# Performance work log

Measured on AMD Instinct MI355X. Metric: run time of the kernel, lower is better.

## Reference

```python
import jax, jax.numpy as jnp
import numpy as np

N = 25600          # total nodes
B = 64             # graphs in batch
NPG = N // B       # nodes per graph (400)
K = 16             # in-degree (regular graph)
E = N * K          # edges
D = 128            # hidden dim = out dim
L = 4              # DGN layers
NUM_ATOM = 128


def _linear_init(key, out_s, in_s):
    lim = 1.0 / np.sqrt(in_s)
    return jax.random.uniform(key, (out_s, in_s), jnp.float32, -lim, lim)


def setup_inputs() -> dict:
    key = jax.random.key(0)
    ks = jax.random.split(key, 16)
    node_feat = jax.random.randint(ks[0], (N,), 0, NUM_ATOM)
    # K-regular in-degree graph, edges intra-graph; dst sorted
    dst = jnp.repeat(jnp.arange(N), K)                       # [E]
    src_local = jax.random.randint(ks[1], (E,), 0, NPG)
    src = (dst // NPG) * NPG + src_local                     # same graph as dst
    eig = jax.random.normal(ks[2], (E, 2), jnp.float32)
    snorm_n = jnp.full((N, 1), 1.0 / np.sqrt(NPG), jnp.float32)
    graph_ids = jnp.arange(N) // NPG
    emb = jax.random.normal(ks[3], (NUM_ATOM, D), jnp.float32) * 0.02
    pre_W = jnp.stack([_linear_init(jax.random.fold_in(ks[4], i), D, 2 * D) for i in range(L)])
    pre_b = jnp.zeros((L, D), jnp.float32)
    post_W = jnp.stack([_linear_init(jax.random.fold_in(ks[5], i), D, 5 * D) for i in range(L)])
    post_b = jnp.zeros((L, D), jnp.float32)
    r_W0 = _linear_init(ks[6], 64, 128); r_b0 = jnp.zeros((64,), jnp.float32)
    r_W1 = _linear_init(ks[7], 32, 64);  r_b1 = jnp.zeros((32,), jnp.float32)
    r_W2 = _linear_init(ks[8], 128, 32); r_b2 = jnp.zeros((128,), jnp.float32)
    return dict(node_feat=node_feat, src=src, dst=dst, eig=eig, snorm_n=snorm_n,
                graph_ids=graph_ids, emb=emb, pre_W=pre_W, pre_b=pre_b,
                post_W=post_W, post_b=post_b, r_W0=r_W0, r_b0=r_b0,
                r_W1=r_W1, r_b1=r_b1, r_W2=r_W2, r_b2=r_b2)


def _dgn_layer(h, src, dst, eig, snorm_n, Wp, bp, Wq, bq):
    n = h.shape[0]
    # pretrans on edges: Linear(cat(h_src, h_dst))  [E, D]
    z2 = jnp.concatenate([h[src], h[dst]], axis=-1)
    e = jnp.einsum('ei,oi->eo', z2, Wp) + bp
    seg_sum = lambda v: jax.ops.segment_sum(v, dst, num_segments=n, indices_are_sorted=True)
    s = seg_sum(e)
    mean = s / K
    mx = jax.ops.segment_max(e, dst, num_segments=n, indices_are_sorted=True)
    # directional aggregator (eig_idx=1)
    w = eig[:, 1]
    denom = seg_sum(jnp.abs(w)) + 1e-8                       # [n]
    ew = w / denom[dst]                                      # [E]
    dir_agg = jnp.abs(seg_sum(e * ew[:, None]) - seg_sum(ew)[:, None] * h)
    agg = jnp.concatenate([h, mean, s, mx, dir_agg], axis=-1)  # [n, 5D]
    hn = jnp.einsum('ni,oi->no', agg, Wq) + bq
    hn = hn * snorm_n           # graph_norm
    hn = jax.nn.relu(hn)
    return h + hn               # residual (in_dim == out_dim)


def reference(node_feat, src, dst, eig, snorm_n, graph_ids, emb,
              pre_W, pre_b, post_W, post_b,
              r_W0, r_b0, r_W1, r_b1, r_W2, r_b2):
    h = emb[node_feat]                                       # AtomEncoder
    for i in range(L):
        h = _dgn_layer(h, src, dst, eig, snorm_n, pre_W[i], pre_b[i], post_W[i], post_b[i])
    # mean_nodes per graph (equal-sized graphs)
    hg = jax.ops.segment_sum(h, graph_ids, num_segments=B, indices_are_sorted=True) / NPG
    y = jax.nn.relu(hg @ r_W0.T + r_b0)
    y = jax.nn.relu(y @ r_W1.T + r_b1)
    return y @ r_W2.T + r_b2                                 # [B, 128]
```

## Files before the change

### kernel.cpp

```cpp
#include <hip/hip_runtime.h>
#include <cstddef>

#define NN 25600
#define BB 64
#define NPG 400
#define KK 16
#define LL 4

typedef _Float16 half_t;
typedef _Float16 h8 __attribute__((ext_vector_type(8)));
typedef _Float16 h4 __attribute__((ext_vector_type(4)));
typedef _Float16 h2 __attribute__((ext_vector_type(2)));
typedef float f32x4 __attribute__((ext_vector_type(4)));

__global__ __launch_bounds__(256) void prep_k(const float* __restrict__ preW,
                                              const float* __restrict__ preb,
                                              const float* __restrict__ postW,
                                              half_t* __restrict__ WpreH,
                                              half_t* __restrict__ WpreL,
                                              float* __restrict__ bpre,
                                              half_t* __restrict__ WpostH,
                                              half_t* __restrict__ WpostL) {
  int idx = blockIdx.x * 256 + threadIdx.x;
  const int n1 = LL * 256 * 128;
  const int n2 = n1 + LL * 256;
  const int n3 = n2 + LL * 128 * 512;
  if (idx < n1) {
    int l = idx / 32768;
    int q = idx % 32768;
    int j = q & 7, lane = (q >> 3) & 63, kc = (q >> 9) & 3, c16 = q >> 11;
    int col = c16 * 16 + (lane & 15);
    int k = kc * 32 + (lane >> 4) * 8 + j;
    float v = (col < 128) ? preW[(size_t)l * 32768 + (size_t)col * 256 + k]
                          : preW[(size_t)l * 32768 + (size_t)(col - 128) * 256 + 128 + k];
    half_t hi = (half_t)v;
    WpreH[idx] = hi;
    WpreL[idx] = (half_t)(v - (float)hi);
  } else if (idx < n2) {
    int r = idx - n1;
    int l = r / 256, o = r % 256;
    bpre[r] = (o < 128) ? 0.f : preb[l * 128 + (o - 128)];
  } else if (idx < n3) {
    int r = idx - n2;
    int l = r / 65536;
    int q = r % 65536;
    int j = q & 7, lane = (q >> 3) & 63, kc = (q >> 9) & 15, c16 = q >> 13;
    int col = c16 * 16 + (lane & 15);
    int k = kc * 32 + (lane >> 4) * 8 + j;
    int jblk = k >> 7, kk = k & 127;
    const float* base = postW + (size_t)l * 128 * 640 + (size_t)col * 640;
    float v;
    if (jblk == 0)      v = base[kk];
    else if (jblk == 1) v = base[128 + kk] * (1.f / 16.f) + base[256 + kk];
    else if (jblk == 2) v = base[384 + kk];
    else                v = base[512 + kk];
    half_t hi = (half_t)v;
    WpostH[r] = hi;
    WpostL[r] = (half_t)(v - (float)hi);
  }
}

__global__ __launch_bounds__(256) void embed_k(const int* __restrict__ nf,
                                               const float* __restrict__ emb,
                                               float* __restrict__ hf,
                                               half_t* __restrict__ Hh,
                                               half_t* __restrict__ Hl) {
  int idx = blockIdx.x * 256 + threadIdx.x;
  int n = idx >> 5;
  int d4 = idx & 31;
  int a = nf[n];
  float4 v = *(const float4*)(emb + (size_t)a * 128 + d4 * 4);
  *(float4*)(hf + (size_t)n * 128 + d4 * 4) = v;
  h4 hi, lo;
  const float* vp = &v.x;
#pragma unroll
  for (int j = 0; j < 4; ++j) {
    half_t h = (half_t)vp[j];
    hi[j] = h;
    lo[j] = (half_t)(vp[j] - (float)h);
  }
  *(h4*)(Hh + (size_t)n * 128 + d4 * 4) = hi;
  *(h4*)(Hl + (size_t)n * 128 + d4 * 4) = lo;
}

__global__ __launch_bounds__(256) void pre_gemm_k(const half_t* __restrict__ Ah_g,
                                                  const half_t* __restrict__ Al_g,
                                                  const half_t* __restrict__ Wh_g,
                                                  const half_t* __restrict__ Wl_g,
                                                  const float* __restrict__ bias,
                                                  float* __restrict__ outF) {
  __shared__ half_t Ahs[64][132];
  __shared__ half_t Als[64][132];
  const int tid = threadIdx.x;
  const int bid = blockIdx.x;
  const int swz = (bid & 7) * 50 + (bid >> 3);
  const int r0 = swz * 64;
  const int by8 = blockIdx.y * 8;
  const int wid = tid >> 6, lane = tid & 63;
  const int wm = wid >> 1, wn = wid & 1;
  const int lr = lane & 15, lk = (lane >> 4) * 8;
  f32x4 acc[2][4] = {};

  {
    const int row = tid >> 2;
#pragma unroll
    for (int s = 0; s < 4; ++s) {
      const int koff = (tid & 3) * 8 + s * 32;
      const size_t g = (size_t)(r0 + row) * 128 + koff;
      *(h8*)&Ahs[row][koff] = *(const h8*)(Ah_g + g);
      *(h8*)&Als[row][koff] = *(const h8*)(Al_g + g);
    }
  }
  __syncthreads();

#pragma unroll
  for (int kc = 0; kc < 4; ++kc) {
    h8 af[2][2];
#pragma unroll
    for (int mi = 0; mi < 2; ++mi) {
      const int r = wm * 32 + mi * 16 + lr;
      af[mi][0] = *(const h8*)&Ahs[r][kc * 32 + lk];
      af[mi][1] = *(const h8*)&Als[r][kc * 32 + lk];
    }
#pragma unroll
    for (int nj = 0; nj < 4; ++nj) {
      const size_t fi = ((size_t)((by8 + wn * 4 + nj) * 4 + kc) * 64 + lane) * 8;
      const h8 b0v = *(const h8*)(Wh_g + fi);
      const h8 b1v = *(const h8*)(Wl_g + fi);
#pragma unroll
      for (int mi = 0; mi < 2; ++mi) {
        acc[mi][nj] = __builtin_amdgcn_mfma_f32_16x16x32_f16(af[mi][0], b0v, acc[mi][nj], 0, 0, 0);
        acc[mi][nj] = __builtin_amdgcn_mfma_f32_16x16x32_f16(af[mi][0], b1v, acc[mi][nj], 0, 0, 0);
        acc[mi][nj] = __builtin_amdgcn_mfma_f32_16x16x32_f16(af[mi][1], b0v, acc[mi][nj], 0, 0, 0);
      }
    }
  }
#pragma unroll
  for (int mi = 0; mi < 2; ++mi) {
    const int rowb = r0 + wm * 32 + mi * 16 + (lane >> 4) * 4;
#pragma unroll
    for (int nj = 0; nj < 4; ++nj) {
      const int col = by8 * 16 + wn * 64 + nj * 16 + lr;
      const float bv = bias[col];
#pragma unroll
      for (int q = 0; q < 4; ++q) {
        outF[(size_t)(rowb + q) * 256 + col] = acc[mi][nj][q] + bv;
      }
    }
  }
}

__global__ __launch_bounds__(256) void agg_post_k(const float* __restrict__ pre,
                                                  const int* __restrict__ src,
                                                  const float* __restrict__ eig,
                                                  const half_t* __restrict__ Hh,
                                                  const half_t* __restrict__ Hl,
                                                  const half_t* __restrict__ Wh,
                                                  const half_t* __restrict__ Wl,
                                                  const float* __restrict__ bias,
                                                  const float* __restrict__ snorm,
                                                  float* __restrict__ Hf,
                                                  half_t* __restrict__ Oh,
                                                  half_t* __restrict__ Ol) {
  __shared__ half_t Ah[16][392];
  __shared__ half_t Al[16][392];
  const int tid = threadIdx.x;
  const int bid = blockIdx.x;
  const int swz = (bid & 7) * 200 + (bid >> 3);
  const int r0 = swz * 16;
  const int wid = tid >> 6, lane = tid & 63;
  const int wn = wid;
  const int lr = lane & 15, lk = (lane >> 4) * 8;

  for (int i = 0; i < 4; ++i) {
    const int lrow = wid * 4 + i;
    const int n = r0 + lrow;
    int sv[KK];
    float wv[KK];
    {
      const int4* sp4 = (const int4*)(src + (size_t)n * KK);
      const float4* ep4 = (const float4*)(eig + (size_t)n * KK * 2);
#pragma unroll
      for (int t = 0; t < 4; ++t) {
        const int4 s4 = sp4[t];
        sv[4 * t + 0] = s4.x;
        sv[4 * t + 1] = s4.y;
        sv[4 * t + 2] = s4.z;
        sv[4 * t + 3] = s4.w;
      }
#pragma unroll
      for (int t = 0; t < 8; ++t) {
        const float4 e4 = ep4[t];
        wv[2 * t + 0] = e4.y;
        wv[2 * t + 1] = e4.w;
      }
    }
    float denom = 0.f;
#pragma unroll
    for (int e = 0; e < KK; ++e) denom += fabsf(wv[e]);
    denom += 1e-8f;
    const float inv = 1.f / denom;
    float sum_ew = 0.f;
#pragma unroll
    for (int e = 0; e < KK; ++e) {
      wv[e] *= inv;
      sum_ew += wv[e];
    }
    float sA0 = 0.f, sA1 = 0.f, wA0 = 0.f, wA1 = 0.f;
    float mA0 = -3.402823466e+38f, mA1 = -3.402823466e+38f;
#pragma unroll
    for (int e = 0; e < KK; ++e) {
      const float2 a = *(const float2*)(pre + (size_t)sv[e] * 256 + 2 * lane);
      sA0 += a.x;
      sA1 += a.y;
      wA0 = fmaf(wv[e], a.x, wA0);
      wA1 = fmaf(wv[e], a.y, wA1);
      mA0 = fmaxf(mA0, a.x);
      mA1 = fmaxf(mA1, a.y);
    }
    const float2 b = *(const float2*)(pre + (size_t)n * 256 + 128 + 2 * lane);
    const float2 hv = *(const float2*)(Hf + (size_t)n * 128 + 2 * lane);
    const int d0 = 2 * lane;
    auto wr2 = [&](int kcol, float v0, float v1) {
      h2 hi, lo;
      hi[0] = (half_t)v0;
      hi[1] = (half_t)v1;
      lo[0] = (half_t)(v0 - (float)hi[0]);
      lo[1] = (half_t)(v1 - (float)hi[1]);
      *(h2*)&Ah[lrow][kcol] = hi;
      *(h2*)&Al[lrow][kcol] = lo;
    };
    wr2(d0, sA0 + 16.f * b.x, sA1 + 16.f * b.y);
    wr2(128 + d0, mA0 + b.x, mA1 + b.y);
    wr2(256 + d0, fabsf(wA0 + sum_ew * (b.x - hv.x)), fabsf(wA1 + sum_ew * (b.y - hv.y)));
  }

  const int frow = r0 + lr;
  h8 afh[4][2];
#pragma unroll
  for (int hc = 0; hc < 4; ++hc) {
    afh[hc][0] = *(const h8*)(Hh + (size_t)frow * 128 + hc * 32 + lk);
    afh[hc][1] = *(const h8*)(Hl + (size_t)frow * 128 + hc * 32 + lk);
  }

  __syncthreads();

  f32x4 acc[2] = {};
#pragma unroll
  for (int kc = 0; kc < 16; ++kc) {
    h8 a0, a1;
    if (kc < 4) {
      a0 = afh[kc & 3][0];
      a1 = afh[kc & 3][1];
    } else {
      a0 = *(const h8*)&Ah[lr][(kc - 4) * 32 + lk];
      a1 = *(const h8*)&Al[lr][(kc - 4) * 32 + lk];
    }
#pragma unroll
    for (int nj = 0; nj < 2; ++nj) {
      const size_t fi = ((size_t)((wn * 2 + nj) * 16 + kc) * 64 + lane) * 8;
      const h8 b0v = *(const h8*)(Wh + fi);
      const h8 b1v = *(const h8*)(Wl + fi);
      acc[nj] = __builtin_amdgcn_mfma_f32_16x16x32_f16(a0, b0v, acc[nj], 0, 0, 0);
      acc[nj] = __builtin_amdgcn_mfma_f32_16x16x32_f16(a0, b1v, acc[nj], 0, 0, 0);
      acc[nj] = __builtin_amdgcn_mfma_f32_16x16x32_f16(a1, b0v, acc[nj], 0, 0, 0);
    }
  }

  const int rowb = r0 + (lane >> 4) * 4;
#pragma unroll
  for (int nj = 0; nj < 2; ++nj) {
    const int col = wn * 32 + nj * 16 + lr;
    const float bv = bias[col];
#pragma unroll
    for (int q = 0; q < 4; ++q) {
      const int r = rowb + q;
      float a = acc[nj][q] + bv;
      a *= snorm[r];
      a = fmaxf(a, 0.f);
      const float hn = Hf[(size_t)r * 128 + col] + a;
      Hf[(size_t)r * 128 + col] = hn;
      const half_t hi = (half_t)hn;
      Oh[(size_t)r * 128 + col] = hi;
      Ol[(size_t)r * 128 + col] = (half_t)(hn - (float)hi);
    }
  }
}

__global__ __launch_bounds__(256) void reduce_mlp_k(const float* __restrict__ h,
                                                    const float* __restrict__ W0, const float* __restrict__ b0,
                                                    const float* __restrict__ W1, const float* __restrict__ b1,
                                                    const float* __restrict__ W2, const float* __restrict__ b2,
                                                    float* __restrict__ out) {
  __shared__ float hgs[128];
  __shared__ float red[128];
  __shared__ float y0s[64];
  __shared__ float y1s[32];
  __shared__ float wb[64 * 130];
  const int g = blockIdx.x;
  const int t = threadIdx.x;
  {
    const int d = t & 127, hf = t >> 7;
    const float* p = h + ((size_t)g * NPG + (size_t)hf * 200) * 128 + d;
    float acc = 0.f;
    for (int i = 0; i < 200; ++i) acc += p[(size_t)i * 128];
    if (hf) red[d] = acc;
    __syncthreads();
    if (!hf) hgs[d] = (acc + red[d]) * (1.f / (float)NPG);
  }
  __syncthreads();
  for (int idx = t; idx < 64 * 128; idx += 256) {
    wb[(idx >> 7) * 130 + (idx & 127)] = W0[idx];
  }
  __syncthreads();
  if (t < 64) {
    float a = b0[t];
    const float* w = &wb[t * 130];
    for (int k = 0; k < 128; ++k) a = fmaf(hgs[k], w[k], a);
    y0s[t] = fmaxf(a, 0.f);
  }
  __syncthreads();
  for (int idx = t; idx < 32 * 64; idx += 256) {
    wb[(idx >> 6) * 66 + (idx & 63)] = W1[idx];
  }
  __syncthreads();
  if (t < 32) {
    float a = b1[t];
    const float* w = &wb[t * 66];
    for (int k = 0; k < 64; ++k) a = fmaf(y0s[k], w[k], a);
    y1s[t] = fmaxf(a, 0.f);
  }
  __syncthreads();
  for (int idx = t; idx < 128 * 32; idx += 256) {
    wb[(idx >> 5) * 34 + (idx & 31)] = W2[idx];
  }
  __syncthreads();
  if (t < 128) {
    float a = b2[t];
    const float* w = &wb[t * 34];
    for (int k = 0; k < 32; ++k) a = fmaf(y1s[k], w[k], a);
    out[(size_t)g * 128 + t] = a;
  }
}

extern "C" void kernel_launch(void* const* d_in, const int* in_sizes, int n_in,
                              void* d_out, int out_size, void* d_ws, size_t ws_size,
                              hipStream_t stream) {
  const int* node_feat = (const int*)d_in[0];
  const int* src = (const int*)d_in[1];
  const float* eig = (const float*)d_in[3];
  const float* snorm = (const float*)d_in[4];
  const float* emb = (const float*)d_in[6];
  const float* preW = (const float*)d_in[7];
  const float* preb = (const float*)d_in[8];
  const float* postW = (const float*)d_in[9];
  const float* postb = (const float*)d_in[10];
  const float* rW0 = (const float*)d_in[11];
  const float* rb0 = (const float*)d_in[12];
  const float* rW1 = (const float*)d_in[13];
  const float* rb1 = (const float*)d_in[14];
  const float* rW2 = (const float*)d_in[15];
  const float* rb2 = (const float*)d_in[16];
  float* out = (float*)d_out;

  half_t* Hh = (half_t*)d_ws;
  half_t* Hl = Hh + (size_t)NN * 128;
  float* Hf = (float*)(Hl + (size_t)NN * 128);
  float* pre = Hf + (size_t)NN * 128;
  half_t* WpreH = (half_t*)(pre + (size_t)NN * 256);
  half_t* WpreL = WpreH + (size_t)LL * 32768;
  half_t* WpostH = WpreL + (size_t)LL * 32768;
  half_t* WpostL = WpostH + (size_t)LL * 65536;
  float* bpre = (float*)(WpostL + (size_t)LL * 65536);

  prep_k<<<1540, 256, 0, stream>>>(preW, preb, postW, WpreH, WpreL, bpre, WpostH, WpostL);
  embed_k<<<(NN * 32) / 256, 256, 0, stream>>>(node_feat, emb, Hf, Hh, Hl);

  for (int l = 0; l < LL; ++l) {
    pre_gemm_k<<<dim3(NN / 64, 2), 256, 0, stream>>>(
        Hh, Hl, WpreH + (size_t)l * 32768, WpreL + (size_t)l * 32768,
        bpre + (size_t)l * 256, pre);
    agg_post_k<<<NN / 16, 256, 0, stream>>>(
        pre, src, eig, Hh, Hl, WpostH + (size_t)l * 65536, WpostL + (size_t)l * 65536,
        postb + (size_t)l * 128, snorm, Hf, Hh, Hl);
  }

  reduce_mlp_k<<<BB, 256, 0, stream>>>(Hf, rW0, rb0, rW1, rb1, rW2, rb2, out);
}
```

Baseline: 266.0 us.

## Fuse dst-half pretrans GEMM into aggregation and drop fp32 hidden buffer

The pre-GEMM now computes only the source-side 128 columns. Each aggregation block computes the destination-side projection for its own 16 rows with MFMA into shared memory, which halves the size of the intermediate edge-projection buffer in global memory. The fp32 copy of the hidden state is also removed: the residual and the readout reconstruct h from the fp16 hi/lo split, which cuts global reads and writes. The cost is extra MFMA work and shared memory in agg_post_k, plus slightly lower precision for the residual state.

```diff
diff --git a/kernel.cpp b/kernel.cpp
--- a/kernel.cpp
+++ b/kernel.cpp
@@ -62,7 +62,6 @@
 
 __global__ __launch_bounds__(256) void embed_k(const int* __restrict__ nf,
                                                const float* __restrict__ emb,
-                                               float* __restrict__ hf,
                                                half_t* __restrict__ Hh,
                                                half_t* __restrict__ Hl) {
   int idx = blockIdx.x * 256 + threadIdx.x;
@@ -70,7 +69,6 @@
   int d4 = idx & 31;
   int a = nf[n];
   float4 v = *(const float4*)(emb + (size_t)a * 128 + d4 * 4);
-  *(float4*)(hf + (size_t)n * 128 + d4 * 4) = v;
   h4 hi, lo;
   const float* vp = &v.x;
 #pragma unroll
@@ -87,15 +85,13 @@
                                                   const half_t* __restrict__ Al_g,
                                                   const half_t* __restrict__ Wh_g,
                                                   const half_t* __restrict__ Wl_g,
-                                                  const float* __restrict__ bias,
-                                                  float* __restrict__ outF) {
+                                                  float* __restrict__ preA) {
   __shared__ half_t Ahs[64][132];
   __shared__ half_t Als[64][132];
   const int tid = threadIdx.x;
   const int bid = blockIdx.x;
   const int swz = (bid & 7) * 50 + (bid >> 3);
   const int r0 = swz * 64;
-  const int by8 = blockIdx.y * 8;
   const int wid = tid >> 6, lane = tid & 63;
   const int wm = wid >> 1, wn = wid & 1;
   const int lr = lane & 15, lk = (lane >> 4) * 8;
@@ -124,7 +120,7 @@
     }
 #pragma unroll
     for (int nj = 0; nj < 4; ++nj) {
-      const size_t fi = ((size_t)((by8 + wn * 4 + nj) * 4 + kc) * 64 + lane) * 8;
+      const size_t fi = ((size_t)((wn * 4 + nj) * 4 + kc) * 64 + lane) * 8;
       const h8 b0v = *(const h8*)(Wh_g + fi);
       const h8 b1v = *(const h8*)(Wl_g + fi);
 #pragma unroll
@@ -140,30 +136,30 @@
     const int rowb = r0 + wm * 32 + mi * 16 + (lane >> 4) * 4;
 #pragma unroll
     for (int nj = 0; nj < 4; ++nj) {
-      const int col = by8 * 16 + wn * 64 + nj * 16 + lr;
-      const float bv = bias[col];
+      const int col = wn * 64 + nj * 16 + lr;
 #pragma unroll
       for (int q = 0; q < 4; ++q) {
-        outF[(size_t)(rowb + q) * 256 + col] = acc[mi][nj][q] + bv;
-      }
-    }
-  }
-}
-
-__global__ __launch_bounds__(256) void agg_post_k(const float* __restrict__ pre,
+        preA[(size_t)(rowb + q) * 128 + col] = acc[mi][nj][q];
+      }
+    }
+  }
+}
+
+__global__ __launch_bounds__(256) void agg_post_k(const float* __restrict__ preA,
                                                   const int* __restrict__ src,
                                                   const float* __restrict__ eig,
-                                                  const half_t* __restrict__ Hh,
-                                                  const half_t* __restrict__ Hl,
+                                                  const half_t* __restrict__ WpHg,
+                                                  const half_t* __restrict__ WpLg,
+                                                  const float* __restrict__ bpre128,
+                                                  half_t* __restrict__ Hh,
+                                                  half_t* __restrict__ Hl,
                                                   const half_t* __restrict__ Wh,
                                                   const half_t* __restrict__ Wl,
                                                   const float* __restrict__ bias,
-                                                  const float* __restrict__ snorm,
-                                                  float* __restrict__ Hf,
-                                                  half_t* __restrict__ Oh,
-                                                  half_t* __restrict__ Ol) {
+                                                  const float* __restrict__ snorm) {
   __shared__ half_t Ah[16][392];
   __shared__ half_t Al[16][392];
+  __shared__ float bsh[16][132];
   const int tid = threadIdx.x;
   const int bid = blockIdx.x;
   const int swz = (bid & 7) * 200 + (bid >> 3);
@@ -171,6 +167,42 @@
   const int wid = tid >> 6, lane = tid & 63;
   const int wn = wid;
   const int lr = lane & 15, lk = (lane >> 4) * 8;
+  const int d0 = 2 * lane;
+
+  const int frow = r0 + lr;
+  h8 afh[4][2];
+#pragma unroll
+  for (int hc = 0; hc < 4; ++hc) {
+    afh[hc][0] = *(const h8*)(Hh + (size_t)frow * 128 + hc * 32 + lk);
+    afh[hc][1] = *(const h8*)(Hl + (size_t)frow * 128 + hc * 32 + lk);
+  }
+
+  {
+    f32x4 bacc[2] = {};
+#pragma unroll
+    for (int kc = 0; kc < 4; ++kc) {
+#pragma unroll
+      for (int nj = 0; nj < 2; ++nj) {
+        const size_t fi = ((size_t)((8 + wn * 2 + nj) * 4 + kc) * 64 + lane) * 8;
+        const h8 b0v = *(const h8*)(WpHg + fi);
+        const h8 b1v = *(const h8*)(WpLg + fi);
+        bacc[nj] = __builtin_amdgcn_mfma_f32_16x16x32_f16(afh[kc][0], b0v, bacc[nj], 0, 0, 0);
+        bacc[nj] = __builtin_amdgcn_mfma_f32_16x16x32_f16(afh[kc][0], b1v, bacc[nj], 0, 0, 0);
+        bacc[nj] = __builtin_amdgcn_mfma_f32_16x16x32_f16(afh[kc][1], b0v, bacc[nj], 0, 0, 0);
+      }
+    }
+    const int rowb = (lane >> 4) * 4;
+#pragma unroll
+    for (int nj = 0; nj < 2; ++nj) {
+      const int col = (wn * 2 + nj) * 16 + lr;
+      const float bv = bpre128[col];
+#pragma unroll
+      for (int q = 0; q < 4; ++q) {
+        bsh[rowb + q][col] = bacc[nj][q] + bv;
+      }
+    }
+  }
+  __syncthreads();
 
   for (int i = 0; i < 4; ++i) {
     const int lrow = wid * 4 + i;
@@ -210,7 +242,7 @@
     float mA0 = -3.402823466e+38f, mA1 = -3.402823466e+38f;
 #pragma unroll
     for (int e = 0; e < KK; ++e) {
-      const float2 a = *(const float2*)(pre + (size_t)sv[e] * 256 + 2 * lane);
+      const float2 a = *(const float2*)(preA + (size_t)sv[e] * 128 + d0);
       sA0 += a.x;
       sA1 += a.y;
       wA0 = fmaf(wv[e], a.x, wA0);
@@ -218,9 +250,11 @@
       mA0 = fmaxf(mA0, a.x);
       mA1 = fmaxf(mA1, a.y);
     }
-    const float2 b = *(const float2*)(pre + (size_t)n * 256 + 128 + 2 * lane);
-    const float2 hv = *(const float2*)(Hf + (size_t)n * 128 + 2 * lane);
-    const int d0 = 2 * lane;
+    const float2 b = {bsh[lrow][d0], bsh[lrow][d0 + 1]};
+    const h2 hh2 = *(const h2*)(Hh + (size_t)n * 128 + d0);
+    const h2 hl2 = *(const h2*)(Hl + (size_t)n * 128 + d0);
+    const float hx = (float)hh2[0] + (float)hl2[0];
+    const float hy = (float)hh2[1] + (float)hl2[1];
     auto wr2 = [&](int kcol, float v0, float v1) {
       h2 hi, lo;
       hi[0] = (half_t)v0;
@@ -232,17 +266,8 @@
     };
     wr2(d0, sA0 + 16.f * b.x, sA1 + 16.f * b.y);
     wr2(128 + d0, mA0 + b.x, mA1 + b.y);
-    wr2(256 + d0, fabsf(wA0 + sum_ew * (b.x - hv.x)), fabsf(wA1 + sum_ew * (b.y - hv.y)));
-  }
-
-  const int frow = r0 + lr;
-  h8 afh[4][2];
-#pragma unroll
-  for (int hc = 0; hc < 4; ++hc) {
-    afh[hc][0] = *(const h8*)(Hh + (size_t)frow * 128 + hc * 32 + lk);
-    afh[hc][1] = *(const h8*)(Hl + (size_t)frow * 128 + hc * 32 + lk);
-  }
-
+    wr2(256 + d0, fabsf(wA0 + sum_ew * (b.x - hx)), fabsf(wA1 + sum_ew * (b.y - hy)));
+  }
   __syncthreads();
 
   f32x4 acc[2] = {};
@@ -278,16 +303,18 @@
       float a = acc[nj][q] + bv;
       a *= snorm[r];
       a = fmaxf(a, 0.f);
-      const float hn = Hf[(size_t)r * 128 + col] + a;
-      Hf[(size_t)r * 128 + col] = hn;
+      const size_t off = (size_t)r * 128 + col;
+      const float hold = (float)Hh[off] + (float)Hl[off];
+      const float hn = hold + a;
       const half_t hi = (half_t)hn;
-      Oh[(size_t)r * 128 + col] = hi;
-      Ol[(size_t)r * 128 + col] = (half_t)(hn - (float)hi);
-    }
-  }
-}
-
-__global__ __launch_bounds__(256) void reduce_mlp_k(const float* __restrict__ h,
+      Hh[off] = hi;
+      Hl[off] = (half_t)(hn - (float)hi);
+    }
+  }
+}
+
+__global__ __launch_bounds__(256) void reduce_mlp_k(const half_t* __restrict__ Hh,
+                                                    const half_t* __restrict__ Hl,
                                                     const float* __restrict__ W0, const float* __restrict__ b0,
                                                     const float* __restrict__ W1, const float* __restrict__ b1,
                                                     const float* __restrict__ W2, const float* __restrict__ b2,
@@ -301,9 +328,12 @@
   const int t = threadIdx.x;
   {
     const int d = t & 127, hf = t >> 7;
-    const float* p = h + ((size_t)g * NPG + (size_t)hf * 200) * 128 + d;
+    const size_t base = ((size_t)g * NPG + (size_t)hf * 200) * 128 + d;
     float acc = 0.f;
-    for (int i = 0; i < 200; ++i) acc += p[(size_t)i * 128];
+    for (int i = 0; i < 200; ++i) {
+      const size_t off = base + (size_t)i * 128;
+      acc += (float)Hh[off] + (float)Hl[off];
+    }
     if (hf) red[d] = acc;
     __syncthreads();
     if (!hf) hgs[d] = (acc + red[d]) * (1.f / (float)NPG);
@@ -365,25 +395,27 @@
 
   half_t* Hh = (half_t*)d_ws;
   half_t* Hl = Hh + (size_t)NN * 128;
-  float* Hf = (float*)(Hl + (size_t)NN * 128);
-  float* pre = Hf + (size_t)NN * 128;
-  half_t* WpreH = (half_t*)(pre + (size_t)NN * 256);
+  float* preA = (float*)(Hl + (size_t)NN * 128);
+  half_t* WpreH = (half_t*)(preA + (size_t)NN * 128);
   half_t* WpreL = WpreH + (size_t)LL * 32768;
   half_t* WpostH = WpreL + (size_t)LL * 32768;
   half_t* WpostL = WpostH + (size_t)LL * 65536;
   float* bpre = (float*)(WpostL + (size_t)LL * 65536);
 
   prep_k<<<1540, 256, 0, stream>>>(preW, preb, postW, WpreH, WpreL, bpre, WpostH, WpostL);
-  embed_k<<<(NN * 32) / 256, 256, 0, stream>>>(node_feat, emb, Hf, Hh, Hl);
+  embed_k<<<(NN * 32) / 256, 256, 0, stream>>>(node_feat, emb, Hh, Hl);
 
   for (int l = 0; l < LL; ++l) {
-    pre_gemm_k<<<dim3(NN / 64, 2), 256, 0, stream>>>(
-        Hh, Hl, WpreH + (size_t)l * 32768, WpreL + (size_t)l * 32768,
-        bpre + (size_t)l * 256, pre);
+    pre_gemm_k<<<NN / 64, 256, 0, stream>>>(
+        Hh, Hl, WpreH + (size_t)l * 32768, WpreL + (size_t)l * 32768, preA);
     agg_post_k<<<NN / 16, 256, 0, stream>>>(
-        pre, src, eig, Hh, Hl, WpostH + (size_t)l * 65536, WpostL + (size_t)l * 65536,
-        postb + (size_t)l * 128, snorm, Hf, Hh, Hl);
-  }
-
-  reduce_mlp_k<<<BB, 256, 0, stream>>>(Hf, rW0, rb0, rW1, rb1, rW2, rb2, out);
-}
+        preA, src, eig,
+        WpreH + (size_t)l * 32768, WpreL + (size_t)l * 32768,
+        bpre + (size_t)l * 256 + 128,
+        Hh, Hl,
+        WpostH + (size_t)l * 65536, WpostL + (size_t)l * 65536,
+        postb + (size_t)l * 128, snorm);
+  }
+
+  reduce_mlp_k<<<BB, 256, 0, stream>>>(Hh, Hl, rW0, rb0, rW1, rb1, rW2, rb2, out);
+}
```

Measured after the change: 280.1 us. 5.3% more time.
